# Optimization experiments

Measured on AMD Instinct MI355X. Metric: run time of the kernel, lower is better.

The kernel has to match this reference:

```python
import jax, jax.numpy as jnp
import numpy as np

T, A, F, E_FEAT = 64, 16, 4, 64
E = F * E_FEAT          # 256 lattice embed dim
H_ENC = 256             # encoder LSTM hidden (per direction)
D_IN = 256              # input token embed dim
DEC_HID = 2 * H_ENC     # decoder hidden = concat(fwd,bwd) encoder hidden
D_ATTN = 256
V_LAT, V_IN = 20000, 100000
NEG = jnp.float32(-1e10)
DEC_LAYERS = 2


def setup_inputs() -> dict:
    key = jax.random.key(0)
    ks = jax.random.split(key, 20)
    def gn(k, shape, scale=0.05):
        return jax.random.normal(k, shape, dtype=jnp.float32) * scale
    inp = {}
    inp['lattice'] = jax.random.randint(ks[0], (1, T, A, F), 0, V_LAT, dtype=jnp.int32)
    inp['analysis_lengths'] = jnp.full((1, T), A, dtype=jnp.int32)
    inp['inputs'] = jax.random.randint(ks[1], (1, T), 0, V_IN, dtype=jnp.int32)
    inp['input_lengths'] = jnp.full((1, 1, 1), T, dtype=jnp.int32)
    inp['gold_indices'] = jax.random.randint(ks[2], (1, T), 0, A, dtype=jnp.int32)
    inp['sos_ids'] = jax.random.randint(ks[3], (F,), 0, V_LAT, dtype=jnp.int32)
    inp['lat_emb_table'] = gn(ks[4], (V_LAT, E_FEAT))
    inp['in_emb_table'] = gn(ks[5], (V_IN, D_IN))
    # encoder biLSTM: 2 layers x 2 directions (PyTorch gate order i,f,g,o)
    inp['enc_Wih0'] = gn(ks[6], (2, 4 * H_ENC, E))
    inp['enc_Whh0'] = gn(ks[7], (2, 4 * H_ENC, H_ENC))
    inp['enc_b0'] = gn(ks[8], (2, 4 * H_ENC))
    inp['enc_Wih1'] = gn(ks[9], (2, 4 * H_ENC, 2 * H_ENC))
    inp['enc_Whh1'] = gn(ks[10], (2, 4 * H_ENC, H_ENC))
    inp['enc_b1'] = gn(ks[11], (2, 4 * H_ENC))
    # decoder LSTM: 2 layers, input = E + D_IN == DEC_HID
    inp['dec_Wih'] = gn(ks[12], (DEC_LAYERS, 4 * DEC_HID, E + D_IN))
    inp['dec_Whh'] = gn(ks[13], (DEC_LAYERS, 4 * DEC_HID, DEC_HID))
    inp['dec_b'] = gn(ks[14], (DEC_LAYERS, 4 * DEC_HID))
    # additive pointer attention
    inp['attn_Wq'] = gn(ks[15], (DEC_HID, D_ATTN))
    inp['attn_Wk'] = gn(ks[16], (DEC_HID, D_ATTN))
    inp['attn_v'] = gn(ks[17], (D_ATTN,))
    return inp


def _lstm_cell(x, h, c, Wih, Whh, b):
    g = x @ Wih.T + h @ Whh.T + b
    i, f, gg, o = jnp.split(g, 4, axis=-1)
    c = jax.nn.sigmoid(f) * c + jax.nn.sigmoid(i) * jnp.tanh(gg)
    h = jax.nn.sigmoid(o) * jnp.tanh(c)
    return h, c


def _lstm_layer(xs, Wih, Whh, b, reverse):
    h0 = jnp.zeros((Whh.shape[-1],), xs.dtype)
    def step(carry, x):
        h, c = _lstm_cell(x, carry[0], carry[1], Wih, Whh, b)
        return (h, c), h
    (hT, cT), ys = jax.lax.scan(step, (h0, h0), xs, reverse=reverse)
    return ys, hT, cT


def reference(lattice, analysis_lengths, inputs, input_lengths, gold_indices, sos_ids,
              lat_emb_table, in_emb_table,
              enc_Wih0, enc_Whh0, enc_b0, enc_Wih1, enc_Whh1, enc_b1,
              dec_Wih, dec_Whh, dec_b, attn_Wq, attn_Wk, attn_v):
    # embed lattice: per-feature lookup, flatten feature embeds -> [1,T,A,E]
    emb_lat = lat_emb_table[lattice].reshape(1, T, A, E)
    # pack full lattice (analysis_lengths == A) into one sequence [T*A, E]
    x = emb_lat[0].reshape(T * A, E)
    # encoder biLSTM layer 0
    yf, hf0, cf0 = _lstm_layer(x, enc_Wih0[0], enc_Whh0[0], enc_b0[0], False)
    yb, hb0, cb0 = _lstm_layer(x, enc_Wih0[1], enc_Whh0[1], enc_b0[1], True)
    y = jnp.concatenate([yf, yb], axis=-1)
    # encoder biLSTM layer 1
    yf, hf1, cf1 = _lstm_layer(y, enc_Wih1[0], enc_Whh1[0], enc_b1[0], False)
    yb, hb1, cb1 = _lstm_layer(y, enc_Wih1[1], enc_Whh1[1], enc_b1[1], True)
    enc = jnp.concatenate([yf, yb], axis=-1).reshape(T, A, DEC_HID)
    # decoder init hidden: concat fwd/bwd final states per layer (matches the
    # view/transpose/reshape in forward_lattice_encode)
    h_dec = jnp.stack([jnp.concatenate([hf0, hb0]), jnp.concatenate([hf1, hb1])])
    c_dec = jnp.stack([jnp.concatenate([cf0, cb0]), jnp.concatenate([cf1, cb1])])
    sos_emb = lat_emb_table[sos_ids].reshape(E)
    tok_emb = in_emb_table[inputs[0]]      # [T, D_IN]
    lat_seq = emb_lat[0]                   # [T, A, E]
    gold = gold_indices[0]                 # [T] teacher forcing
    alens = analysis_lengths[0]            # [T]
    col = jnp.arange(A)

    def step(carry, xs):
        h, c, prev = carry
        enc_t, tok_t, lat_t, g_t, len_t = xs
        inp_t = jnp.concatenate([prev, tok_t])   # [E + D_IN]
        hs, cs = [], []
        for l in range(DEC_LAYERS):
            hl, cl = _lstm_cell(inp_t, h[l], c[l], dec_Wih[l], dec_Whh[l], dec_b[l])
            hs.append(hl); cs.append(cl)
            inp_t = hl
        att = jnp.tanh(enc_t @ attn_Wk + inp_t @ attn_Wq) @ attn_v   # [A]
        scores = jnp.where(col < len_t, att, NEG)
        return (jnp.stack(hs), jnp.stack(cs), lat_t[g_t]), scores

    _, scores = jax.lax.scan(step, (h_dec, c_dec, sos_emb), (enc, tok_emb, lat_seq, gold, alens))
    return scores[None]  # [1, T, A]
```

## Files before the change

kernel.cpp:

```cpp
#include <hip/hip_runtime.h>
#include <math.h>

#define T_STEPS 64
#define A_DIM   16
#define SEQ     1024
#define HE      256
#define DH      512
#define GE      1024
#define GD      2048

typedef _Float16 h2_t __attribute__((ext_vector_type(2)));

__device__ __forceinline__ float sigf(float x) { return 1.f / (1.f + __expf(-x)); }
__device__ __forceinline__ float tanh_fast(float x) {
    float e = __expf(-2.f * x);
    return (1.f - e) / (1.f + e);
}

__device__ __forceinline__ float fdot2f(h2_t a, h2_t b, float c) {
#if defined(__has_builtin) && __has_builtin(__builtin_amdgcn_fdot2)
    return __builtin_amdgcn_fdot2(a, b, c, false);
#else
    return c + (float)a.x * (float)b.x + (float)a.y * (float)b.y;
#endif
}

__device__ __forceinline__ float poll_comm(const float* p) {
    float v;
    do {
        v = __hip_atomic_load(p, __ATOMIC_RELAXED, __HIP_MEMORY_SCOPE_AGENT);
    } while (v == 0.f);
    return v - 4.0f;
}

__device__ __forceinline__ void post_comm(float* p, float h) {
    __hip_atomic_store(p, h + 4.0f, __ATOMIC_RELAXED, __HIP_MEMORY_SCOPE_AGENT);
}

__global__ void k_embed(const int* __restrict__ lattice, const int* __restrict__ inputs,
                        const int* __restrict__ gold, const int* __restrict__ sos,
                        const float* __restrict__ lat_emb, const float* __restrict__ in_emb,
                        float* __restrict__ x, float* __restrict__ decin)
{
    int idx = blockIdx.x * 256 + threadIdx.x;
    if (idx < SEQ * 256) {
        int row = idx >> 8, e = idx & 255;
        int f = e >> 6, eo = e & 63;
        int id = lattice[row * 4 + f];
        x[idx] = lat_emb[id * 64 + eo];
    } else {
        int k = idx - SEQ * 256;
        if (k < T_STEPS * 512) {
            int t = k >> 9, d = k & 511;
            float val;
            if (d < 256) {
                int f = d >> 6, eo = d & 63;
                int id = (t == 0) ? sos[f]
                                  : lattice[(((t - 1) * A_DIM) + gold[t - 1]) * 4 + f];
                val = lat_emb[id * 64 + eo];
            } else {
                val = in_emb[inputs[t] * 256 + (d - 256)];
            }
            decin[k] = val;
        }
    }
}

__global__ __launch_bounds__(256) void k_gemm(
    const float* __restrict__ A, int lda, long sA,
    const float* __restrict__ B, int ldbn, int ldbk, long sB,
    const float* __restrict__ bias, int sBias,
    float* __restrict__ C, int ldc, long sC,
    int M, int N, int K)
{
    int b = blockIdx.z;
    A += b * sA; B += b * sB; C += b * sC;
    if (bias) bias += (long)b * sBias;
    int n0 = blockIdx.x * 64, m0 = blockIdx.y * 64;
    __shared__ float As[64][17];
    __shared__ float Bs[64][17];
    int tid = threadIdx.x;
    int tn = tid & 15, tm = tid >> 4;
    float acc[4][4] = {};
    int lk = tid & 15, lr = tid >> 4;
    for (int k0 = 0; k0 < K; k0 += 16) {
#pragma unroll
        for (int i = 0; i < 4; i++) {
            int row = lr + i * 16;
            int am = m0 + row;
            As[row][lk] = (am < M) ? A[(long)am * lda + k0 + lk] : 0.f;
            int bn = n0 + row;
            Bs[row][lk] = (bn < N) ? B[(long)bn * ldbn + (long)(k0 + lk) * ldbk] : 0.f;
        }
        __syncthreads();
#pragma unroll
        for (int k = 0; k < 16; k++) {
            float av[4], bv[4];
#pragma unroll
            for (int i = 0; i < 4; i++) av[i] = As[tm * 4 + i][k];
#pragma unroll
            for (int j = 0; j < 4; j++) bv[j] = Bs[tn * 4 + j][k];
#pragma unroll
            for (int i = 0; i < 4; i++)
#pragma unroll
                for (int j = 0; j < 4; j++) acc[i][j] += av[i] * bv[j];
        }
        __syncthreads();
    }
#pragma unroll
    for (int i = 0; i < 4; i++) {
        int m = m0 + tm * 4 + i;
        if (m >= M) continue;
#pragma unroll
        for (int j = 0; j < 4; j++) {
            int n = n0 + tn * 4 + j;
            if (n < N) C[(long)m * ldc + n] = acc[i][j] + (bias ? bias[n] : 0.f);
        }
    }
}

__global__ __launch_bounds__(256, 1) void k_rec_enc(
    const float* __restrict__ pre,
    const float* __restrict__ Whh,
    float* __restrict__ y,
    float* __restrict__ hfin,
    float* __restrict__ cfin,
    float* __restrict__ comm)
{
    const int tid = threadIdx.x, bid = blockIdx.x;
    const int r = bid & 3, dir = bid >> 2;
    const bool fwd = (dir == 0);
    const int jj = tid & 63, j = r * 64 + jj;
    const int row = (tid >> 6) * HE + j;
    const float* pre_d = pre + (long)dir * SEQ * GE;
    float* comm_d = comm + (long)dir * SEQ * HE;

    h2_t w2[128];
    {
        const float4* wr = (const float4*)(Whh + (long)dir * GE * HE + (long)row * HE);
#pragma unroll
        for (int i = 0; i < 64; i++) {
            float4 v = wr[i];
            w2[2 * i]     = h2_t{(_Float16)v.x, (_Float16)v.y};
            w2[2 * i + 1] = h2_t{(_Float16)v.z, (_Float16)v.w};
        }
    }

    __shared__ __align__(16) _Float16 hsArr[HE];
    __shared__ float gl[256];
    hsArr[tid] = (_Float16)0.f;
    __syncthreads();

    float c = 0.f, h_cur = 0.f;
    float pre_cur = pre_d[(long)(fwd ? 0 : SEQ - 1) * GE + row];

    for (int s = 0; s < SEQ; s++) {
        const int t = fwd ? s : SEQ - 1 - s;
        float acc = 0.f;
        const float4* hv = (const float4*)hsArr;
#pragma unroll
        for (int kk = 0; kk < 32; kk++) {
            float4 blk = hv[kk];
            const h2_t* hp = (const h2_t*)&blk;
            acc = fdot2f(w2[4 * kk + 0], hp[0], acc);
            acc = fdot2f(w2[4 * kk + 1], hp[1], acc);
            acc = fdot2f(w2[4 * kk + 2], hp[2], acc);
            acc = fdot2f(w2[4 * kk + 3], hp[3], acc);
        }
        gl[tid] = pre_cur + acc;
        if (s + 1 < SEQ) pre_cur = pre_d[(long)(fwd ? t + 1 : t - 1) * GE + row];
        __syncthreads();
        if (tid < 64) {
            float gi = gl[jj], gf = gl[64 + jj], gg = gl[128 + jj], go = gl[192 + jj];
            c = sigf(gf) * c + sigf(gi) * tanh_fast(gg);
            h_cur = sigf(go) * tanh_fast(c);
            post_comm(&comm_d[(long)t * HE + j], h_cur);
            y[(long)t * 512 + dir * HE + j] = h_cur;
            hsArr[j] = (_Float16)h_cur;
        }
        if (s + 1 < SEQ && tid < 192) {
            int idx = (r * 64 + 64 + tid) & 255;
            hsArr[idx] = (_Float16)poll_comm(&comm_d[(long)t * HE + idx]);
        }
        __syncthreads();
    }
    if (tid < 64) {
        hfin[dir * HE + j] = h_cur;
        cfin[dir * HE + j] = c;
    }
}

__global__ __launch_bounds__(256, 1) void k_rec_dec(
    const float* __restrict__ pre,
    const float* __restrict__ Whh,
    const float* __restrict__ hinit,
    const float* __restrict__ cinit,
    float* __restrict__ hseq,
    float* __restrict__ comm)
{
    const int tid = threadIdx.x, r = blockIdx.x;
    const int kh = tid >> 7, rem = tid & 127;
    const int q = rem >> 5, jj = rem & 31;
    const int row = q * DH + r * 32 + jj;
    const int k0 = kh * 256;

    h2_t w2[128];
    {
        const float4* wr = (const float4*)(Whh + (long)row * DH + k0);
#pragma unroll
        for (int i = 0; i < 64; i++) {
            float4 v = wr[i];
            w2[2 * i]     = h2_t{(_Float16)v.x, (_Float16)v.y};
            w2[2 * i + 1] = h2_t{(_Float16)v.z, (_Float16)v.w};
        }
    }

    __shared__ __align__(16) _Float16 hsArr[DH];
    __shared__ float part[256];
    __shared__ float gate[128];
    hsArr[tid] = (_Float16)hinit[tid];
    hsArr[tid + 256] = (_Float16)hinit[tid + 256];
    float c = (tid < 32) ? cinit[r * 32 + tid] : 0.f;
    float pre_cur = (tid < 128) ? pre[row] : 0.f;
    float h_cur = 0.f;
    __syncthreads();

    for (int s = 0; s < T_STEPS; s++) {
        float acc = 0.f;
        const float4* hv = (const float4*)(hsArr + k0);
#pragma unroll
        for (int kk = 0; kk < 32; kk++) {
            float4 blk = hv[kk];
            const h2_t* hp = (const h2_t*)&blk;
            acc = fdot2f(w2[4 * kk + 0], hp[0], acc);
            acc = fdot2f(w2[4 * kk + 1], hp[1], acc);
            acc = fdot2f(w2[4 * kk + 2], hp[2], acc);
            acc = fdot2f(w2[4 * kk + 3], hp[3], acc);
        }
        part[tid] = acc;
        __syncthreads();
        if (tid < 128) {
            float g = part[tid] + part[tid + 128] + pre_cur;
            if (s + 1 < T_STEPS) pre_cur = pre[(long)(s + 1) * GD + row];
            gate[tid] = g;
        }
        __syncthreads();
        if (tid < 32) {
            int jg = r * 32 + tid;
            float gi = gate[tid], gf = gate[32 + tid], gg = gate[64 + tid], go = gate[96 + tid];
            c = sigf(gf) * c + sigf(gi) * tanh_fast(gg);
            h_cur = sigf(go) * tanh_fast(c);
            post_comm(&comm[(long)s * DH + jg], h_cur);
            hseq[(long)s * DH + jg] = h_cur;
            hsArr[jg] = (_Float16)h_cur;
        }
        if (s + 1 < T_STEPS) {
            if (tid < 224) {
                int idx = (r * 32 + 32 + tid) & 511;
                hsArr[idx] = (_Float16)poll_comm(&comm[(long)s * DH + idx]);
            }
            {
                int idx = (r * 32 + 256 + tid) & 511;
                hsArr[idx] = (_Float16)poll_comm(&comm[(long)s * DH + idx]);
            }
        }
        __syncthreads();
    }
}

__global__ void k_attn(const float* __restrict__ encK, const float* __restrict__ qs,
                       const float* __restrict__ v, const int* __restrict__ alens,
                       float* __restrict__ out)
{
    int t = blockIdx.x;
    int tid = threadIdx.x;
    int wave = tid >> 6, lane = tid & 63;
    int len = alens[t];
    const float* qt = qs + t * 256;
    for (int a = wave; a < A_DIM; a += 4) {
        const float* ek = encK + (long)(t * A_DIM + a) * 256;
        float sum = 0.f;
#pragma unroll
        for (int e = 0; e < 4; e++) {
            int d = lane * 4 + e;
            sum += v[d] * tanhf(ek[d] + qt[d]);
        }
        for (int off = 32; off; off >>= 1) sum += __shfl_down(sum, off, 64);
        if (lane == 0) out[t * A_DIM + a] = (a < len) ? sum : -1e10f;
    }
}

extern "C" void kernel_launch(void* const* d_in, const int* in_sizes, int n_in,
                              void* d_out, int out_size, void* d_ws, size_t ws_size,
                              hipStream_t stream)
{
    (void)in_sizes; (void)n_in; (void)out_size; (void)ws_size;
    const int*   lattice = (const int*)d_in[0];
    const int*   alens   = (const int*)d_in[1];
    const int*   inputs  = (const int*)d_in[2];
    const int*   gold    = (const int*)d_in[4];
    const int*   sos     = (const int*)d_in[5];
    const float* lat_emb = (const float*)d_in[6];
    const float* in_emb  = (const float*)d_in[7];
    const float* Wih0    = (const float*)d_in[8];
    const float* Whh0    = (const float*)d_in[9];
    const float* b0      = (const float*)d_in[10];
    const float* Wih1    = (const float*)d_in[11];
    const float* Whh1    = (const float*)d_in[12];
    const float* b1      = (const float*)d_in[13];
    const float* dWih    = (const float*)d_in[14];
    const float* dWhh    = (const float*)d_in[15];
    const float* db      = (const float*)d_in[16];
    const float* Wq      = (const float*)d_in[17];
    const float* Wk      = (const float*)d_in[18];
    const float* av      = (const float*)d_in[19];
    float* out = (float*)d_out;
    float* ws  = (float*)d_ws;

    float* comm  = ws;
    float* commD = ws + 524288;
    float* xbuf  = ws + 589824;
    float* dpre  = xbuf;
    float* h0seq = xbuf + 131072;
    float* h1seq = xbuf + 163840;
    float* qseq  = xbuf + 196608;
    float* pre   = ws + 851968;
    float* y0    = ws + 2949120;
    float* hdec  = ws + 3473408;
    float* cdec  = ws + 3474432;
    float* decin = ws + 3475456;
    float* encK  = ws + 3508224;

    hipMemsetAsync(ws, 0, (524288 + 65536) * sizeof(float), stream);

    k_embed<<<1152, 256, 0, stream>>>(lattice, inputs, gold, sos, lat_emb, in_emb, xbuf, decin);

    k_gemm<<<dim3(16, 16, 2), 256, 0, stream>>>(
        xbuf, 256, 0L, Wih0, 256, 1, (long)GE * 256, b0, GE,
        pre, GE, (long)SEQ * GE, SEQ, GE, 256);
    k_rec_enc<<<8, 256, 0, stream>>>(pre, Whh0, y0, hdec, cdec, comm);

    hipMemsetAsync(comm, 0, 524288 * sizeof(float), stream);

    k_gemm<<<dim3(16, 16, 2), 256, 0, stream>>>(
        y0, 512, 0L, Wih1, 512, 1, (long)GE * 512, b1, GE,
        pre, GE, (long)SEQ * GE, SEQ, GE, 512);
    k_rec_enc<<<8, 256, 0, stream>>>(pre, Whh1, y0, hdec + 512, cdec + 512, comm);

    k_gemm<<<dim3(4, 16, 1), 256, 0, stream>>>(
        y0, 512, 0L, Wk, 1, 256, 0L, nullptr, 0,
        encK, 256, 0L, SEQ, 256, 512);

    k_gemm<<<dim3(32, 1, 1), 256, 0, stream>>>(
        decin, 512, 0L, dWih, 512, 1, 0L, db, 0,
        dpre, GD, 0L, T_STEPS, GD, 512);
    k_rec_dec<<<16, 256, 0, stream>>>(dpre, dWhh, hdec, cdec, h0seq, commD);

    k_gemm<<<dim3(32, 1, 1), 256, 0, stream>>>(
        h0seq, 512, 0L, dWih + (long)GD * 512, 512, 1, 0L, db + GD, 0,
        dpre, GD, 0L, T_STEPS, GD, 512);
    k_rec_dec<<<16, 256, 0, stream>>>(dpre, dWhh + (long)GD * 512, hdec + 512, cdec + 512,
                                      h1seq, commD + 32768);

    k_gemm<<<dim3(4, 1, 1), 256, 0, stream>>>(
        h1seq, 512, 0L, Wq, 1, 256, 0L, nullptr, 0,
        qseq, 256, 0L, T_STEPS, 256, 512);

    k_attn<<<64, 256, 0, stream>>>(encK, qseq, av, alens, out);
}
```

Before: 3.959 ms.

## Run each encoder LSTM direction in one workgroup, drop cross-block polling

The encoder recurrence now uses one 512-thread workgroup per direction instead of four cooperating blocks. Each thread holds two gate rows of Whh in fp16 registers, so the per-step hidden-state exchange through global memory polling disappears and the comm buffer and its memset go away. The decoder recurrence likewise shrinks from 16 blocks to 4 blocks of 512 threads, each owning 128 hidden units, which cuts inter-block communication and removes one barrier per step. The cost is twice the register-resident weights per thread and half as many parallel lanes per row, which lengthens the serial dot-product work each step.

```diff
diff --git a/kernel.cpp b/kernel.cpp
--- a/kernel.cpp
+++ b/kernel.cpp
@@ -119,78 +119,92 @@
     }
 }
 
-__global__ __launch_bounds__(256, 1) void k_rec_enc(
+__global__ __launch_bounds__(512, 1) void k_rec_enc(
     const float* __restrict__ pre,
     const float* __restrict__ Whh,
     float* __restrict__ y,
     float* __restrict__ hfin,
-    float* __restrict__ cfin,
-    float* __restrict__ comm)
-{
-    const int tid = threadIdx.x, bid = blockIdx.x;
-    const int r = bid & 3, dir = bid >> 2;
+    float* __restrict__ cfin)
+{
+    const int tid = threadIdx.x;
+    const int dir = blockIdx.x;
     const bool fwd = (dir == 0);
-    const int jj = tid & 63, j = r * 64 + jj;
-    const int row = (tid >> 6) * HE + j;
+    const int j = tid & 255;
+    const int half = tid >> 8;
+    const int row_a = half * 256 + j;
+    const int row_b = row_a + 512;
     const float* pre_d = pre + (long)dir * SEQ * GE;
-    float* comm_d = comm + (long)dir * SEQ * HE;
-
-    h2_t w2[128];
+
+    h2_t wa[128], wb[128];
     {
-        const float4* wr = (const float4*)(Whh + (long)dir * GE * HE + (long)row * HE);
+        const float4* ra = (const float4*)(Whh + (long)dir * GE * HE + (long)row_a * HE);
+        const float4* rb = (const float4*)(Whh + (long)dir * GE * HE + (long)row_b * HE);
 #pragma unroll
         for (int i = 0; i < 64; i++) {
-            float4 v = wr[i];
-            w2[2 * i]     = h2_t{(_Float16)v.x, (_Float16)v.y};
-            w2[2 * i + 1] = h2_t{(_Float16)v.z, (_Float16)v.w};
+            float4 va = ra[i], vb = rb[i];
+            wa[2 * i]     = h2_t{(_Float16)va.x, (_Float16)va.y};
+            wa[2 * i + 1] = h2_t{(_Float16)va.z, (_Float16)va.w};
+            wb[2 * i]     = h2_t{(_Float16)vb.x, (_Float16)vb.y};
+            wb[2 * i + 1] = h2_t{(_Float16)vb.z, (_Float16)vb.w};
+        }
+#pragma unroll
+        for (int i = 0; i < 128; i++) {
+            asm volatile("" : "+v"(wa[i]));
+            asm volatile("" : "+v"(wb[i]));
         }
     }
 
     __shared__ __align__(16) _Float16 hsArr[HE];
-    __shared__ float gl[256];
-    hsArr[tid] = (_Float16)0.f;
+    __shared__ float gl[GE];
+    if (tid < 256) hsArr[tid] = (_Float16)0.f;
     __syncthreads();
 
     float c = 0.f, h_cur = 0.f;
-    float pre_cur = pre_d[(long)(fwd ? 0 : SEQ - 1) * GE + row];
+    const int t0 = fwd ? 0 : SEQ - 1;
+    float pa = pre_d[(long)t0 * GE + row_a];
+    float pb = pre_d[(long)t0 * GE + row_b];
 
     for (int s = 0; s < SEQ; s++) {
         const int t = fwd ? s : SEQ - 1 - s;
-        float acc = 0.f;
+        float a0 = 0, a1 = 0, b0 = 0, b1 = 0;
         const float4* hv = (const float4*)hsArr;
 #pragma unroll
         for (int kk = 0; kk < 32; kk++) {
             float4 blk = hv[kk];
             const h2_t* hp = (const h2_t*)&blk;
-            acc = fdot2f(w2[4 * kk + 0], hp[0], acc);
-            acc = fdot2f(w2[4 * kk + 1], hp[1], acc);
-            acc = fdot2f(w2[4 * kk + 2], hp[2], acc);
-            acc = fdot2f(w2[4 * kk + 3], hp[3], acc);
-        }
-        gl[tid] = pre_cur + acc;
-        if (s + 1 < SEQ) pre_cur = pre_d[(long)(fwd ? t + 1 : t - 1) * GE + row];
-        __syncthreads();
-        if (tid < 64) {
-            float gi = gl[jj], gf = gl[64 + jj], gg = gl[128 + jj], go = gl[192 + jj];
+            a0 = fdot2f(wa[4 * kk + 0], hp[0], a0);
+            a1 = fdot2f(wa[4 * kk + 1], hp[1], a1);
+            a0 = fdot2f(wa[4 * kk + 2], hp[2], a0);
+            a1 = fdot2f(wa[4 * kk + 3], hp[3], a1);
+            b0 = fdot2f(wb[4 * kk + 0], hp[0], b0);
+            b1 = fdot2f(wb[4 * kk + 1], hp[1], b1);
+            b0 = fdot2f(wb[4 * kk + 2], hp[2], b0);
+            b1 = fdot2f(wb[4 * kk + 3], hp[3], b1);
+        }
+        gl[row_a] = pa + (a0 + a1);
+        gl[row_b] = pb + (b0 + b1);
+        if (s + 1 < SEQ) {
+            int tn = fwd ? t + 1 : t - 1;
+            pa = pre_d[(long)tn * GE + row_a];
+            pb = pre_d[(long)tn * GE + row_b];
+        }
+        __syncthreads();
+        if (tid < 256) {
+            float gi = gl[j], gf = gl[256 + j], gg = gl[512 + j], go = gl[768 + j];
             c = sigf(gf) * c + sigf(gi) * tanh_fast(gg);
             h_cur = sigf(go) * tanh_fast(c);
-            post_comm(&comm_d[(long)t * HE + j], h_cur);
-            y[(long)t * 512 + dir * HE + j] = h_cur;
             hsArr[j] = (_Float16)h_cur;
-        }
-        if (s + 1 < SEQ && tid < 192) {
-            int idx = (r * 64 + 64 + tid) & 255;
-            hsArr[idx] = (_Float16)poll_comm(&comm_d[(long)t * HE + idx]);
-        }
-        __syncthreads();
-    }
-    if (tid < 64) {
-        hfin[dir * HE + j] = h_cur;
-        cfin[dir * HE + j] = c;
-    }
-}
-
-__global__ __launch_bounds__(256, 1) void k_rec_dec(
+            y[(long)t * 512 + dir * 256 + j] = h_cur;
+        }
+        __syncthreads();
+    }
+    if (tid < 256) {
+        hfin[dir * 256 + j] = h_cur;
+        cfin[dir * 256 + j] = c;
+    }
+}
+
+__global__ __launch_bounds__(512, 1) void k_rec_dec(
     const float* __restrict__ pre,
     const float* __restrict__ Whh,
     const float* __restrict__ hinit,
@@ -198,71 +212,86 @@
     float* __restrict__ hseq,
     float* __restrict__ comm)
 {
-    const int tid = threadIdx.x, r = blockIdx.x;
-    const int kh = tid >> 7, rem = tid & 127;
-    const int q = rem >> 5, jj = rem & 31;
-    const int row = q * DH + r * 32 + jj;
-    const int k0 = kh * 256;
-
-    h2_t w2[128];
+    const int tid = threadIdx.x, b = blockIdx.x;
+    const int jj = tid & 127;
+    const int p = tid >> 7;
+    const int half = p & 1, gb = p >> 1;
+    const int j_own = b * 128 + jj;
+    const int r1 = gb * 512 + j_own;
+    const int r2 = (gb + 2) * 512 + j_own;
+    const int k0 = half * 256;
+
+    h2_t w1[128], w2[128];
     {
-        const float4* wr = (const float4*)(Whh + (long)row * DH + k0);
+        const float4* ra = (const float4*)(Whh + (long)r1 * DH + k0);
+        const float4* rb = (const float4*)(Whh + (long)r2 * DH + k0);
 #pragma unroll
         for (int i = 0; i < 64; i++) {
-            float4 v = wr[i];
-            w2[2 * i]     = h2_t{(_Float16)v.x, (_Float16)v.y};
-            w2[2 * i + 1] = h2_t{(_Float16)v.z, (_Float16)v.w};
+            float4 va = ra[i], vb = rb[i];
+            w1[2 * i]     = h2_t{(_Float16)va.x, (_Float16)va.y};
+            w1[2 * i + 1] = h2_t{(_Float16)va.z, (_Float16)va.w};
+            w2[2 * i]     = h2_t{(_Float16)vb.x, (_Float16)vb.y};
+            w2[2 * i + 1] = h2_t{(_Float16)vb.z, (_Float16)vb.w};
+        }
+#pragma unroll
+        for (int i = 0; i < 128; i++) {
+            asm volatile("" : "+v"(w1[i]));
+            asm volatile("" : "+v"(w2[i]));
         }
     }
 
     __shared__ __align__(16) _Float16 hsArr[DH];
-    __shared__ float part[256];
-    __shared__ float gate[128];
+    __shared__ float part[1024];
     hsArr[tid] = (_Float16)hinit[tid];
-    hsArr[tid + 256] = (_Float16)hinit[tid + 256];
-    float c = (tid < 32) ? cinit[r * 32 + tid] : 0.f;
-    float pre_cur = (tid < 128) ? pre[row] : 0.f;
+    float c = (tid < 128) ? cinit[j_own] : 0.f;
     float h_cur = 0.f;
+    float p0 = 0.f, p1 = 0.f, p2 = 0.f, p3 = 0.f;
+    if (tid < 128) {
+        p0 = pre[0 * 512 + j_own];
+        p1 = pre[1 * 512 + j_own];
+        p2 = pre[2 * 512 + j_own];
+        p3 = pre[3 * 512 + j_own];
+    }
     __syncthreads();
 
     for (int s = 0; s < T_STEPS; s++) {
-        float acc = 0.f;
+        float a0 = 0, a1 = 0, b0 = 0, b1 = 0;
         const float4* hv = (const float4*)(hsArr + k0);
 #pragma unroll
         for (int kk = 0; kk < 32; kk++) {
             float4 blk = hv[kk];
             const h2_t* hp = (const h2_t*)&blk;
-            acc = fdot2f(w2[4 * kk + 0], hp[0], acc);
-            acc = fdot2f(w2[4 * kk + 1], hp[1], acc);
-            acc = fdot2f(w2[4 * kk + 2], hp[2], acc);
-            acc = fdot2f(w2[4 * kk + 3], hp[3], acc);
-        }
-        part[tid] = acc;
+            a0 = fdot2f(w1[4 * kk + 0], hp[0], a0);
+            a1 = fdot2f(w1[4 * kk + 1], hp[1], a1);
+            a0 = fdot2f(w1[4 * kk + 2], hp[2], a0);
+            a1 = fdot2f(w1[4 * kk + 3], hp[3], a1);
+            b0 = fdot2f(w2[4 * kk + 0], hp[0], b0);
+            b1 = fdot2f(w2[4 * kk + 1], hp[1], b1);
+            b0 = fdot2f(w2[4 * kk + 2], hp[2], b0);
+            b1 = fdot2f(w2[4 * kk + 3], hp[3], b1);
+        }
+        part[(gb * 2 + half) * 128 + jj]       = a0 + a1;
+        part[((gb + 2) * 2 + half) * 128 + jj] = b0 + b1;
         __syncthreads();
         if (tid < 128) {
-            float g = part[tid] + part[tid + 128] + pre_cur;
-            if (s + 1 < T_STEPS) pre_cur = pre[(long)(s + 1) * GD + row];
-            gate[tid] = g;
-        }
-        __syncthreads();
-        if (tid < 32) {
-            int jg = r * 32 + tid;
-            float gi = gate[tid], gf = gate[32 + tid], gg = gate[64 + tid], go = gate[96 + tid];
+            float gi = part[0 * 128 + jj] + part[1 * 128 + jj] + p0;
+            float gf = part[2 * 128 + jj] + part[3 * 128 + jj] + p1;
+            float gg = part[4 * 128 + jj] + part[5 * 128 + jj] + p2;
+            float go = part[6 * 128 + jj] + part[7 * 128 + jj] + p3;
+            if (s + 1 < T_STEPS) {
+                p0 = pre[(long)(s + 1) * GD + 0 * 512 + j_own];
+                p1 = pre[(long)(s + 1) * GD + 1 * 512 + j_own];
+                p2 = pre[(long)(s + 1) * GD + 2 * 512 + j_own];
+                p3 = pre[(long)(s + 1) * GD + 3 * 512 + j_own];
+            }
             c = sigf(gf) * c + sigf(gi) * tanh_fast(gg);
             h_cur = sigf(go) * tanh_fast(c);
-            post_comm(&comm[(long)s * DH + jg], h_cur);
-            hseq[(long)s * DH + jg] = h_cur;
-            hsArr[jg] = (_Float16)h_cur;
-        }
-        if (s + 1 < T_STEPS) {
-            if (tid < 224) {
-                int idx = (r * 32 + 32 + tid) & 511;
-                hsArr[idx] = (_Float16)poll_comm(&comm[(long)s * DH + idx]);
-            }
-            {
-                int idx = (r * 32 + 256 + tid) & 511;
-                hsArr[idx] = (_Float16)poll_comm(&comm[(long)s * DH + idx]);
-            }
+            post_comm(&comm[(long)s * DH + j_own], h_cur);
+            hseq[(long)s * DH + j_own] = h_cur;
+            hsArr[j_own] = (_Float16)h_cur;
+        } else if (s + 1 < T_STEPS) {
+            int idx = (b * 128 + 128 + (tid - 128)) & 511;
+            hsArr[idx] = (_Float16)poll_comm(&comm[(long)s * DH + idx]);
         }
         __syncthreads();
     }
@@ -317,35 +346,32 @@
     float* out = (float*)d_out;
     float* ws  = (float*)d_ws;
 
-    float* comm  = ws;
-    float* commD = ws + 524288;
-    float* xbuf  = ws + 589824;
-    float* dpre  = xbuf;
-    float* h0seq = xbuf + 131072;
-    float* h1seq = xbuf + 163840;
-    float* qseq  = xbuf + 196608;
-    float* pre   = ws + 851968;
-    float* y0    = ws + 2949120;
-    float* hdec  = ws + 3473408;
-    float* cdec  = ws + 3474432;
-    float* decin = ws + 3475456;
-    float* encK  = ws + 3508224;
-
-    hipMemsetAsync(ws, 0, (524288 + 65536) * sizeof(float), stream);
+    float* commD = ws;
+    float* xbuf  = ws + 65536;
+    float* pre   = ws + 327680;
+    float* y0    = ws + 2424832;
+    float* hdec  = ws + 2949120;
+    float* cdec  = ws + 2950144;
+    float* decin = ws + 2951168;
+    float* encK  = ws + 2983936;
+    float* dpre  = ws + 3246080;
+    float* h0seq = ws + 3377152;
+    float* h1seq = ws + 3409920;
+    float* qseq  = ws + 3442688;
+
+    hipMemsetAsync(commD, 0, 65536 * sizeof(float), stream);
 
     k_embed<<<1152, 256, 0, stream>>>(lattice, inputs, gold, sos, lat_emb, in_emb, xbuf, decin);
 
     k_gemm<<<dim3(16, 16, 2), 256, 0, stream>>>(
         xbuf, 256, 0L, Wih0, 256, 1, (long)GE * 256, b0, GE,
         pre, GE, (long)SEQ * GE, SEQ, GE, 256);
-    k_rec_enc<<<8, 256, 0, stream>>>(pre, Whh0, y0, hdec, cdec, comm);
-
-    hipMemsetAsync(comm, 0, 524288 * sizeof(float), stream);
+    k_rec_enc<<<2, 512, 0, stream>>>(pre, Whh0, y0, hdec, cdec);
 
     k_gemm<<<dim3(16, 16, 2), 256, 0, stream>>>(
         y0, 512, 0L, Wih1, 512, 1, (long)GE * 512, b1, GE,
         pre, GE, (long)SEQ * GE, SEQ, GE, 512);
-    k_rec_enc<<<8, 256, 0, stream>>>(pre, Whh1, y0, hdec + 512, cdec + 512, comm);
+    k_rec_enc<<<2, 512, 0, stream>>>(pre, Whh1, y0, hdec + 512, cdec + 512);
 
     k_gemm<<<dim3(4, 16, 1), 256, 0, stream>>>(
         y0, 512, 0L, Wk, 1, 256, 0L, nullptr, 0,
@@ -354,13 +380,13 @@
     k_gemm<<<dim3(32, 1, 1), 256, 0, stream>>>(
         decin, 512, 0L, dWih, 512, 1, 0L, db, 0,
         dpre, GD, 0L, T_STEPS, GD, 512);
-    k_rec_dec<<<16, 256, 0, stream>>>(dpre, dWhh, hdec, cdec, h0seq, commD);
+    k_rec_dec<<<4, 512, 0, stream>>>(dpre, dWhh, hdec, cdec, h0seq, commD);
 
     k_gemm<<<dim3(32, 1, 1), 256, 0, stream>>>(
         h0seq, 512, 0L, dWih + (long)GD * 512, 512, 1, 0L, db + GD, 0,
         dpre, GD, 0L, T_STEPS, GD, 512);
-    k_rec_dec<<<16, 256, 0, stream>>>(dpre, dWhh + (long)GD * 512, hdec + 512, cdec + 512,
-                                      h1seq, commD + 32768);
+    k_rec_dec<<<4, 512, 0, stream>>>(dpre, dWhh + (long)GD * 512, hdec + 512, cdec + 512,
+                                     h1seq, commD + 32768);
 
     k_gemm<<<dim3(4, 1, 1), 256, 0, stream>>>(
         h1seq, 512, 0L, Wq, 1, 256, 0L, nullptr, 0,
```

New measurement: 9.413 ms. +137.8%, slower.

## Run each encoder LSTM direction in one 1024-thread block without cross-block polling

Applied to the files above, without the earlier changes.

The encoder recurrence moves from 4 cooperating blocks per direction, which exchange h through global-memory atomics and polling, to a single 1024-thread workgroup per direction. Each workgroup splits the K dimension four ways and reduces partial sums through shared memory. Whh is pre-converted to packed fp16 by a new k_cvt kernel, so each thread holds its 4x32 weight slices in registers. This removes the per-step inter-block communication latency and the large comm memset. The cost is only 2 active CUs, with a shared-memory reduction and two block barriers every step, plus 128 packed registers per thread under 1024-thread launch bounds.

```diff
diff --git a/kernel.cpp b/kernel.cpp
--- a/kernel.cpp
+++ b/kernel.cpp
@@ -35,6 +35,15 @@
 
 __device__ __forceinline__ void post_comm(float* p, float h) {
     __hip_atomic_store(p, h + 4.0f, __ATOMIC_RELAXED, __HIP_MEMORY_SCOPE_AGENT);
+}
+
+__global__ void k_cvt(const float* __restrict__ src, unsigned int* __restrict__ dst, int n)
+{
+    int i = blockIdx.x * 256 + threadIdx.x;
+    if (i < n) {
+        h2_t h; h.x = (_Float16)src[2 * i]; h.y = (_Float16)src[2 * i + 1];
+        dst[i] = *(unsigned int*)&h;
+    }
 }
 
 __global__ void k_embed(const int* __restrict__ lattice, const int* __restrict__ inputs,
@@ -119,74 +128,99 @@
     }
 }
 
-__global__ __launch_bounds__(256, 1) void k_rec_enc(
+__global__ __launch_bounds__(1024, 4) void k_rec_enc(
     const float* __restrict__ pre,
-    const float* __restrict__ Whh,
-    float* __restrict__ y,
-    float* __restrict__ hfin,
-    float* __restrict__ cfin,
-    float* __restrict__ comm)
-{
-    const int tid = threadIdx.x, bid = blockIdx.x;
-    const int r = bid & 3, dir = bid >> 2;
+    const unsigned int* w2,
+    float* y,
+    float* hfin,
+    float* cfin)
+{
+    const int tid = threadIdx.x;
+    const int dir = blockIdx.x;
     const bool fwd = (dir == 0);
-    const int jj = tid & 63, j = r * 64 + jj;
-    const int row = (tid >> 6) * HE + j;
+    const int j  = tid & 255;
+    const int kq = tid >> 8;
     const float* pre_d = pre + (long)dir * SEQ * GE;
-    float* comm_d = comm + (long)dir * SEQ * HE;
-
-    h2_t w2[128];
+
+    h2_t w[4][32];
     {
-        const float4* wr = (const float4*)(Whh + (long)dir * GE * HE + (long)row * HE);
-#pragma unroll
-        for (int i = 0; i < 64; i++) {
-            float4 v = wr[i];
-            w2[2 * i]     = h2_t{(_Float16)v.x, (_Float16)v.y};
-            w2[2 * i + 1] = h2_t{(_Float16)v.z, (_Float16)v.w};
+        const float4* wp = (const float4*)w2;
+#pragma unroll
+        for (int g = 0; g < 4; g++) {
+            long base = ((long)dir * 1024 + g * 256 + j) * 32 + kq * 8;
+#pragma unroll
+            for (int i = 0; i < 8; i++) {
+                float4 v = wp[base + i];
+                const h2_t* hv = (const h2_t*)&v;
+                w[g][i * 4 + 0] = hv[0];
+                w[g][i * 4 + 1] = hv[1];
+                w[g][i * 4 + 2] = hv[2];
+                w[g][i * 4 + 3] = hv[3];
+            }
         }
     }
 
     __shared__ __align__(16) _Float16 hsArr[HE];
-    __shared__ float gl[256];
-    hsArr[tid] = (_Float16)0.f;
+    __shared__ float part[16 * 256];
+    if (tid < 256) hsArr[tid] = (_Float16)0.f;
+
+    float c = 0.f, h_cur = 0.f;
+    float p0 = 0.f, p1 = 0.f, p2 = 0.f, p3 = 0.f;
+    if (tid < 256) {
+        long t0 = fwd ? 0 : SEQ - 1;
+        p0 = pre_d[t0 * GE + 0 * 256 + j];
+        p1 = pre_d[t0 * GE + 1 * 256 + j];
+        p2 = pre_d[t0 * GE + 2 * 256 + j];
+        p3 = pre_d[t0 * GE + 3 * 256 + j];
+    }
     __syncthreads();
-
-    float c = 0.f, h_cur = 0.f;
-    float pre_cur = pre_d[(long)(fwd ? 0 : SEQ - 1) * GE + row];
 
     for (int s = 0; s < SEQ; s++) {
         const int t = fwd ? s : SEQ - 1 - s;
-        float acc = 0.f;
-        const float4* hv = (const float4*)hsArr;
-#pragma unroll
-        for (int kk = 0; kk < 32; kk++) {
-            float4 blk = hv[kk];
-            const h2_t* hp = (const h2_t*)&blk;
-            acc = fdot2f(w2[4 * kk + 0], hp[0], acc);
-            acc = fdot2f(w2[4 * kk + 1], hp[1], acc);
-            acc = fdot2f(w2[4 * kk + 2], hp[2], acc);
-            acc = fdot2f(w2[4 * kk + 3], hp[3], acc);
-        }
-        gl[tid] = pre_cur + acc;
-        if (s + 1 < SEQ) pre_cur = pre_d[(long)(fwd ? t + 1 : t - 1) * GE + row];
-        __syncthreads();
-        if (tid < 64) {
-            float gi = gl[jj], gf = gl[64 + jj], gg = gl[128 + jj], go = gl[192 + jj];
+        float4 hb[8];
+        const float4* hv4 = (const float4*)(hsArr + kq * 64);
+#pragma unroll
+        for (int i = 0; i < 8; i++) hb[i] = hv4[i];
+        const h2_t* hh = (const h2_t*)hb;
+        float a0 = 0, a1 = 0, a2 = 0, a3 = 0;
+#pragma unroll
+        for (int k = 0; k < 32; k++) {
+            a0 = fdot2f(w[0][k], hh[k], a0);
+            a1 = fdot2f(w[1][k], hh[k], a1);
+            a2 = fdot2f(w[2][k], hh[k], a2);
+            a3 = fdot2f(w[3][k], hh[k], a3);
+        }
+        part[(0 * 4 + kq) * 256 + j] = a0;
+        part[(1 * 4 + kq) * 256 + j] = a1;
+        part[(2 * 4 + kq) * 256 + j] = a2;
+        part[(3 * 4 + kq) * 256 + j] = a3;
+        __syncthreads();
+        if (tid < 256) {
+            float gi = p0 + ((part[ 0 * 256 + j] + part[ 1 * 256 + j]) +
+                             (part[ 2 * 256 + j] + part[ 3 * 256 + j]));
+            float gf = p1 + ((part[ 4 * 256 + j] + part[ 5 * 256 + j]) +
+                             (part[ 6 * 256 + j] + part[ 7 * 256 + j]));
+            float gg = p2 + ((part[ 8 * 256 + j] + part[ 9 * 256 + j]) +
+                             (part[10 * 256 + j] + part[11 * 256 + j]));
+            float go = p3 + ((part[12 * 256 + j] + part[13 * 256 + j]) +
+                             (part[14 * 256 + j] + part[15 * 256 + j]));
+            if (s + 1 < SEQ) {
+                long tn = fwd ? t + 1 : t - 1;
+                p0 = pre_d[tn * GE + 0 * 256 + j];
+                p1 = pre_d[tn * GE + 1 * 256 + j];
+                p2 = pre_d[tn * GE + 2 * 256 + j];
+                p3 = pre_d[tn * GE + 3 * 256 + j];
+            }
             c = sigf(gf) * c + sigf(gi) * tanh_fast(gg);
             h_cur = sigf(go) * tanh_fast(c);
-            post_comm(&comm_d[(long)t * HE + j], h_cur);
-            y[(long)t * 512 + dir * HE + j] = h_cur;
             hsArr[j] = (_Float16)h_cur;
-        }
-        if (s + 1 < SEQ && tid < 192) {
-            int idx = (r * 64 + 64 + tid) & 255;
-            hsArr[idx] = (_Float16)poll_comm(&comm_d[(long)t * HE + idx]);
-        }
-        __syncthreads();
-    }
-    if (tid < 64) {
-        hfin[dir * HE + j] = h_cur;
-        cfin[dir * HE + j] = c;
+            y[(long)t * 512 + dir * 256 + j] = h_cur;
+        }
+        __syncthreads();
+    }
+    if (tid < 256) {
+        hfin[dir * 256 + j] = h_cur;
+        cfin[dir * 256 + j] = c;
     }
 }
 
@@ -317,35 +351,35 @@
     float* out = (float*)d_out;
     float* ws  = (float*)d_ws;
 
-    float* comm  = ws;
-    float* commD = ws + 524288;
-    float* xbuf  = ws + 589824;
-    float* dpre  = xbuf;
-    float* h0seq = xbuf + 131072;
-    float* h1seq = xbuf + 163840;
-    float* qseq  = xbuf + 196608;
-    float* pre   = ws + 851968;
-    float* y0    = ws + 2949120;
-    float* hdec  = ws + 3473408;
-    float* cdec  = ws + 3474432;
-    float* decin = ws + 3475456;
-    float* encK  = ws + 3508224;
-
-    hipMemsetAsync(ws, 0, (524288 + 65536) * sizeof(float), stream);
+    float* commD = ws;
+    unsigned int* wcvt = (unsigned int*)(ws + 65536);
+    float* xbuf  = ws + 327680;
+    float* pre   = ws + 589824;
+    float* y0    = ws + 2686976;
+    float* hdec  = ws + 3211264;
+    float* cdec  = ws + 3212288;
+    float* decin = ws + 3213312;
+    float* encK  = ws + 3246080;
+    float* dpre  = ws + 3508224;
+    float* h0seq = ws + 3639296;
+    float* h1seq = ws + 3672064;
+    float* qseq  = ws + 3704832;
+
+    hipMemsetAsync(commD, 0, 65536 * sizeof(float), stream);
 
     k_embed<<<1152, 256, 0, stream>>>(lattice, inputs, gold, sos, lat_emb, in_emb, xbuf, decin);
 
+    k_cvt<<<1024, 256, 0, stream>>>(Whh0, wcvt, 262144);
     k_gemm<<<dim3(16, 16, 2), 256, 0, stream>>>(
         xbuf, 256, 0L, Wih0, 256, 1, (long)GE * 256, b0, GE,
         pre, GE, (long)SEQ * GE, SEQ, GE, 256);
-    k_rec_enc<<<8, 256, 0, stream>>>(pre, Whh0, y0, hdec, cdec, comm);
-
-    hipMemsetAsync(comm, 0, 524288 * sizeof(float), stream);
-
+    k_rec_enc<<<2, 1024, 0, stream>>>(pre, wcvt, y0, hdec, cdec);
+
+    k_cvt<<<1024, 256, 0, stream>>>(Whh1, wcvt, 262144);
     k_gemm<<<dim3(16, 16, 2), 256, 0, stream>>>(
         y0, 512, 0L, Wih1, 512, 1, (long)GE * 512, b1, GE,
         pre, GE, (long)SEQ * GE, SEQ, GE, 512);
-    k_rec_enc<<<8, 256, 0, stream>>>(pre, Whh1, y0, hdec + 512, cdec + 512, comm);
+    k_rec_enc<<<2, 1024, 0, stream>>>(pre, wcvt, y0, hdec + 512, cdec + 512);
 
     k_gemm<<<dim3(4, 16, 1), 256, 0, stream>>>(
         y0, 512, 0L, Wk, 1, 256, 0L, nullptr, 0,
```

Result: slower. 11.49 ms (+190.3%).
